# Kernel tuning notes

Hardware: AMD Instinct MI355X
Metric: run time of the kernel (lower is better)

The kernel has to match this reference:

```python
import jax, jax.numpy as jnp
import numpy as np

NEG_INF = -10000.0
ALPHA = 0.2      # LeakyReLU slope
EPS = 1e-5       # LayerNorm eps
B, N, D = 8, 2048, 128


def setup_inputs() -> dict:
    key = jax.random.key(0)
    ks = jax.random.split(key, 8)
    x = jax.random.normal(ks[0], (B, N, D), dtype=jnp.float32)
    adj_bool = jax.random.randint(ks[1], (B, N, N), 0, 2, dtype=jnp.int32)
    node_mask = jax.random.randint(ks[2], (B, N), 0, 2, dtype=jnp.int32)
    s = 1.0 / np.sqrt(D)
    W = jax.random.uniform(ks[3], (D, D), jnp.float32, -s, s)    # fc weight (in->out)
    a_l = jax.random.uniform(ks[4], (D,), jnp.float32, -s, s)    # attn_l weight
    a_r = jax.random.uniform(ks[5], (D,), jnp.float32, -s, s)    # attn_r weight
    gamma = jnp.ones((D,), jnp.float32)                          # LayerNorm weight
    beta = jnp.zeros((D,), jnp.float32)                          # LayerNorm bias
    return {"x": x, "adj_bool": adj_bool, "node_mask": node_mask,
            "W": W, "a_l": a_l, "a_r": a_r, "gamma": gamma, "beta": beta}


def reference(x, adj_bool, node_mask, W, a_l, a_r, gamma, beta):
    m = node_mask.astype(x.dtype)[..., None]           # [B,N,1]
    x = x * m
    h = jnp.einsum('bnd,de->bne', x, W)                # [B,N,D]
    e_l = jnp.einsum('bnd,d->bn', h, a_l)              # [B,N]
    e_r = jnp.einsum('bnd,d->bn', h, a_r)              # [B,N]
    e = e_l[:, :, None] + e_r[:, None, :]              # [B,N,N]
    e = jnp.where(e > 0, e, ALPHA * e)                 # LeakyReLU
    pair = (node_mask[:, :, None] * node_mask[:, None, :]) > 0
    allowed = (adj_bool > 0) & pair
    e = jnp.where(allowed, e, NEG_INF)
    attn = jax.nn.softmax(e, axis=-1)                  # finite (NEG_INF fill), nan_to_num is a no-op
    out = jnp.einsum('bij,bjd->bid', attn, h)          # dropout in eval mode = identity
    out = (out + x) * m                                # residual (ind==outd), then node mask
    mu = jnp.mean(out, axis=-1, keepdims=True)
    var = jnp.var(out, axis=-1, keepdims=True)
    out = (out - mu) * jax.lax.rsqrt(var + EPS) * gamma + beta
    return out
```

## Files before the change

### kernel.cpp

```cpp
#include <hip/hip_runtime.h>
#include <stdint.h>


#define BB 8
#define NN 2048
#define DD 128
#define GAT_NEG_INF -10000.0f
#define LN_EPS 1e-5f

typedef __attribute__((ext_vector_type(8))) short short8;
typedef __attribute__((ext_vector_type(4))) float f32x4;

__device__ __forceinline__ unsigned pk_bf16(float a, float b) {
    unsigned ua = __float_as_uint(a); ua += 0x7FFFu + ((ua >> 16) & 1u);
    unsigned ub = __float_as_uint(b); ub += 0x7FFFu + ((ub >> 16) & 1u);
    return (ua >> 16) | (ub & 0xFFFF0000u);
}
__device__ __forceinline__ unsigned short bf16_rtn(float a) {
    unsigned ua = __float_as_uint(a);
    return (unsigned short)((ua + 0x7FFFu + ((ua >> 16) & 1u)) >> 16);
}

__global__ void prep_wt(const float* __restrict__ W,
                        unsigned short* __restrict__ WThi,
                        unsigned short* __restrict__ WTlo)
{
    int idx = blockIdx.x * 256 + threadIdx.x;
    int k = idx >> 7, n = idx & 127;
    float w = W[idx];
    unsigned short hi = bf16_rtn(w);
    float hif = __uint_as_float((unsigned)hi << 16);
    WThi[n * DD + k] = hi;
    WTlo[n * DD + k] = bf16_rtn(w - hif);
}

__global__ __launch_bounds__(256) void fc_kernel(
    const float* __restrict__ x, const int* __restrict__ mask,
    const unsigned short* __restrict__ WThi, const unsigned short* __restrict__ WTlo,
    const float* __restrict__ a_l, const float* __restrict__ a_r,
    unsigned short* __restrict__ hT, float* __restrict__ el, float* __restrict__ er)
{
    const int t    = threadIdx.x;
    const int wv   = t >> 6;
    const int lane = t & 63;
    const int col  = lane & 15;
    const int grp  = lane >> 4;
    const int b    = blockIdx.x & 7;
    const int it   = blockIdx.x >> 3;
    const int i0   = it * 64 + wv * 16;

    const float* xrow = x + ((size_t)(b * NN + i0 + col)) * DD + grp * 8;
    const float  mm   = (float)mask[b * NN + i0 + col];

    f32x4 acc[8];
#pragma unroll
    for (int nb = 0; nb < 8; ++nb) acc[nb] = (f32x4)0.f;

    union AU { unsigned u[4]; short8 v; };
    union BU { int4 q; short8 v; };

#pragma unroll
    for (int ks = 0; ks < 4; ++ks) {
        float4 xa = *(const float4*)(xrow + ks * 32);
        float4 xb = *(const float4*)(xrow + ks * 32 + 4);
        float xv[8] = {xa.x, xa.y, xa.z, xa.w, xb.x, xb.y, xb.z, xb.w};
        unsigned short hi[8]; float lo[8];
#pragma unroll
        for (int u = 0; u < 8; ++u) {
            float v = xv[u] * mm;
            hi[u] = bf16_rtn(v);
            lo[u] = v - __uint_as_float((unsigned)hi[u] << 16);
        }
        AU Ahi, Alo;
#pragma unroll
        for (int j = 0; j < 4; ++j) {
            Ahi.u[j] = (unsigned)hi[2 * j] | ((unsigned)hi[2 * j + 1] << 16);
            Alo.u[j] = pk_bf16(lo[2 * j], lo[2 * j + 1]);
        }
#pragma unroll
        for (int nb = 0; nb < 8; ++nb) {
            BU Bhi, Blo;
            Bhi.q = *(const int4*)(WThi + (nb * 16 + col) * DD + ks * 32 + grp * 8);
            Blo.q = *(const int4*)(WTlo + (nb * 16 + col) * DD + ks * 32 + grp * 8);
            acc[nb] = __builtin_amdgcn_mfma_f32_16x16x32_bf16(Ahi.v, Bhi.v, acc[nb], 0, 0, 0);
            acc[nb] = __builtin_amdgcn_mfma_f32_16x16x32_bf16(Alo.v, Bhi.v, acc[nb], 0, 0, 0);
            acc[nb] = __builtin_amdgcn_mfma_f32_16x16x32_bf16(Ahi.v, Blo.v, acc[nb], 0, 0, 0);
        }
    }

    float sl[4] = {0.f, 0.f, 0.f, 0.f}, sr[4] = {0.f, 0.f, 0.f, 0.f};
#pragma unroll
    for (int nb = 0; nb < 8; ++nb) {
        float alv = a_l[nb * 16 + col];
        float arv = a_r[nb * 16 + col];
#pragma unroll
        for (int reg = 0; reg < 4; ++reg) {
            sl[reg] += acc[nb][reg] * alv;
            sr[reg] += acc[nb][reg] * arv;
        }
    }
#pragma unroll
    for (int off = 1; off < 16; off <<= 1)
#pragma unroll
        for (int reg = 0; reg < 4; ++reg) {
            sl[reg] += __shfl_xor(sl[reg], off, 64);
            sr[reg] += __shfl_xor(sr[reg], off, 64);
        }
    if (col == 0) {
#pragma unroll
        for (int reg = 0; reg < 4; ++reg) {
            el[b * NN + i0 + grp * 4 + reg] = sl[reg];
            er[b * NN + i0 + grp * 4 + reg] = sr[reg];
        }
    }

#pragma unroll
    for (int nb = 0; nb < 8; ++nb) {
        unsigned p01 = pk_bf16(acc[nb][0], acc[nb][1]);
        unsigned p23 = pk_bf16(acc[nb][2], acc[nb][3]);
        *(uint2*)(hT + ((size_t)(b * DD + nb * 16 + col)) * NN + i0 + grp * 4) =
            make_uint2(p01, p23);
    }
}

__global__ __launch_bounds__(256, 4) void attn_kernel(
    const float* __restrict__ x, const int* __restrict__ adj,
    const int* __restrict__ mask, const unsigned short* __restrict__ hT,
    const float* __restrict__ el, const float* __restrict__ er,
    const float* __restrict__ gamma, const float* __restrict__ beta,
    float* __restrict__ outp)
{
    __shared__ __align__(16) float macc[4][16][132];
    __shared__ float mls[4][16][2];

    const int t    = threadIdx.x;
    const int wv   = t >> 6;
    const int lane = t & 63;
    const int row  = lane & 15;
    const int grp  = lane >> 4;
    const int b    = blockIdx.x & 7;
    const int it   = blockIdx.x >> 3;
    const int i0   = it * 16;
    const int gi   = i0 + row;
    const int j0   = wv * 512;

    const float el_r = el[b * NN + gi];
    const int   mi   = mask[b * NN + gi];
    const int*  adj_row = adj + ((size_t)(b * NN + gi)) * NN + j0;
    const float* er_w = er + b * NN + j0;
    const int*   mk_w = mask + b * NN + j0;
    const unsigned short* hT_b = hT + (size_t)b * DD * NN;

    f32x4 acc[8];
#pragma unroll
    for (int nb = 0; nb < 8; ++nb) acc[nb] = (f32x4)0.f;
    float m_run = -3.0e38f, l_run = 0.f;

    int4 pa0, pa1, pa2, pa3;
    float4 pe0, pe1, pe2, pe3;
    int4 pq0, pq1, pq2, pq3;

    auto load_meta = [&](int jt) {
        const int jb = jt * 64 + grp * 8;
        pa0 = *(const int4*)(adj_row + jb);
        pa1 = *(const int4*)(adj_row + jb + 4);
        pa2 = *(const int4*)(adj_row + jb + 32);
        pa3 = *(const int4*)(adj_row + jb + 36);
        pe0 = *(const float4*)(er_w + jb);
        pe1 = *(const float4*)(er_w + jb + 4);
        pe2 = *(const float4*)(er_w + jb + 32);
        pe3 = *(const float4*)(er_w + jb + 36);
        pq0 = *(const int4*)(mk_w + jb);
        pq1 = *(const int4*)(mk_w + jb + 4);
        pq2 = *(const int4*)(mk_w + jb + 32);
        pq3 = *(const int4*)(mk_w + jb + 36);
    };
    load_meta(0);

    union BU { int4 q; short8 v; };
    union AU { unsigned u[4]; short8 v; };

#pragma unroll 1
    for (int jt = 0; jt < 8; ++jt) {
        int4 a0 = pa0, a1 = pa1, a2 = pa2, a3 = pa3;
        float4 e0 = pe0, e1 = pe1, e2 = pe2, e3 = pe3;
        int4 q0 = pq0, q1 = pq1, q2 = pq2, q3 = pq3;
        load_meta(jt < 7 ? jt + 1 : jt);

        BU bf[16];
        {
            const int jb = j0 + jt * 64 + grp * 8;
#pragma unroll
            for (int s = 0; s < 2; ++s)
#pragma unroll
                for (int nb = 0; nb < 8; ++nb)
                    bf[s * 8 + nb].q = *(const int4*)(hT_b
                        + (size_t)(nb * 16 + row) * NN + jb + s * 32);
        }

        int   av[16] = {a0.x,a0.y,a0.z,a0.w, a1.x,a1.y,a1.z,a1.w,
                        a2.x,a2.y,a2.z,a2.w, a3.x,a3.y,a3.z,a3.w};
        int   qv[16] = {q0.x,q0.y,q0.z,q0.w, q1.x,q1.y,q1.z,q1.w,
                        q2.x,q2.y,q2.z,q2.w, q3.x,q3.y,q3.z,q3.w};
        float ev[16] = {e0.x,e0.y,e0.z,e0.w, e1.x,e1.y,e1.z,e1.w,
                        e2.x,e2.y,e2.z,e2.w, e3.x,e3.y,e3.z,e3.w};
        float ss[16];
        float tmax = -3.0e38f;
#pragma unroll
        for (int u = 0; u < 16; ++u) {
            float e = el_r + ev[u];
            e = fmaxf(e, 0.2f * e);
            bool ok = (av[u] & qv[u] & mi) != 0;
            ss[u] = ok ? e : GAT_NEG_INF;
            tmax = fmaxf(tmax, ss[u]);
        }
        tmax = fmaxf(tmax, __shfl_xor(tmax, 16, 64));
        tmax = fmaxf(tmax, __shfl_xor(tmax, 32, 64));
        float m_new = fmaxf(m_run, tmax);
        float al    = __expf(m_run - m_new);
        float p[16];
        float psum = 0.f;
#pragma unroll
        for (int u = 0; u < 16; ++u) {
            p[u] = __expf(ss[u] - m_new);
            psum += p[u];
        }
        psum += __shfl_xor(psum, 16, 64);
        psum += __shfl_xor(psum, 32, 64);
        l_run = l_run * al + psum;
        m_run = m_new;

        float alr[4];
#pragma unroll
        for (int reg = 0; reg < 4; ++reg) alr[reg] = __shfl(al, grp * 4 + reg, 64);
#pragma unroll
        for (int nb = 0; nb < 8; ++nb) {
            acc[nb][0] *= alr[0]; acc[nb][1] *= alr[1];
            acc[nb][2] *= alr[2]; acc[nb][3] *= alr[3];
        }

        AU A0, A1;
#pragma unroll
        for (int k = 0; k < 4; ++k) {
            A0.u[k] = pk_bf16(p[2 * k],     p[2 * k + 1]);
            A1.u[k] = pk_bf16(p[8 + 2 * k], p[8 + 2 * k + 1]);
        }
#pragma unroll
        for (int nb = 0; nb < 8; ++nb)
            acc[nb] = __builtin_amdgcn_mfma_f32_16x16x32_bf16(A0.v, bf[nb].v, acc[nb], 0, 0, 0);
#pragma unroll
        for (int nb = 0; nb < 8; ++nb)
            acc[nb] = __builtin_amdgcn_mfma_f32_16x16x32_bf16(A1.v, bf[8 + nb].v, acc[nb], 0, 0, 0);
    }

    if (grp == 0) { mls[wv][row][0] = m_run; mls[wv][row][1] = l_run; }
#pragma unroll
    for (int nb = 0; nb < 8; ++nb)
#pragma unroll
        for (int reg = 0; reg < 4; ++reg)
            macc[wv][grp * 4 + reg][nb * 16 + row] = acc[nb][reg];
    __syncthreads();

    const float g0  = gamma[2 * lane], g1 = gamma[2 * lane + 1];
    const float be0 = beta[2 * lane],  be1 = beta[2 * lane + 1];
#pragma unroll
    for (int q = 0; q < 4; ++q) {
        const int r  = wv * 4 + q;
        const int gir = i0 + r;
        float m0 = mls[0][r][0], m1 = mls[1][r][0], m2 = mls[2][r][0], m3 = mls[3][r][0];
        float m_f = fmaxf(fmaxf(m0, m1), fmaxf(m2, m3));
        float sc0 = __expf(m0 - m_f), sc1 = __expf(m1 - m_f);
        float sc2 = __expf(m2 - m_f), sc3 = __expf(m3 - m_f);
        float l_f = mls[0][r][1] * sc0 + mls[1][r][1] * sc1
                  + mls[2][r][1] * sc2 + mls[3][r][1] * sc3;
        float inv = 1.0f / l_f;
        float2 v0 = *(const float2*)&macc[0][r][2 * lane];
        float2 v1 = *(const float2*)&macc[1][r][2 * lane];
        float2 v2 = *(const float2*)&macc[2][r][2 * lane];
        float2 v3 = *(const float2*)&macc[3][r][2 * lane];
        float ox = v0.x * sc0 + v1.x * sc1 + v2.x * sc2 + v3.x * sc3;
        float oy = v0.y * sc0 + v1.y * sc1 + v2.y * sc2 + v3.y * sc3;

        float mq = (float)mask[b * NN + gir];
        float2 xv = *(const float2*)(x + ((size_t)(b * NN + gir)) * DD + 2 * lane);
        float w0 = (ox * inv + xv.x) * mq;
        float w1 = (oy * inv + xv.y) * mq;

        float s1 = w0 + w1, s2 = w0 * w0 + w1 * w1;
#pragma unroll
        for (int off = 32; off; off >>= 1) {
            s1 += __shfl_xor(s1, off, 64);
            s2 += __shfl_xor(s2, off, 64);
        }
        float mu  = s1 * (1.0f / DD);
        float var = s2 * (1.0f / DD) - mu * mu;
        float rsd = rsqrtf(var + LN_EPS);
        *(float2*)(outp + ((size_t)(b * NN + gir)) * DD + 2 * lane) =
            make_float2((w0 - mu) * rsd * g0 + be0, (w1 - mu) * rsd * g1 + be1);
    }
}

extern "C" void kernel_launch(void* const* d_in, const int* in_sizes, int n_in,
                              void* d_out, int out_size, void* d_ws, size_t ws_size,
                              hipStream_t stream) {
    const float* x     = (const float*)d_in[0];
    const int*   adj   = (const int*)d_in[1];
    const int*   maskp = (const int*)d_in[2];
    const float* W     = (const float*)d_in[3];
    const float* a_l   = (const float*)d_in[4];
    const float* a_r   = (const float*)d_in[5];
    const float* gamma = (const float*)d_in[6];
    const float* beta  = (const float*)d_in[7];
    float*       outp  = (float*)d_out;

    unsigned short* hT = (unsigned short*)d_ws;
    float* el = (float*)(hT + (size_t)BB * DD * NN);
    float* er = el + (size_t)BB * NN;
    unsigned short* WThi = (unsigned short*)(er + (size_t)BB * NN);
    unsigned short* WTlo = WThi + DD * DD;

    prep_wt<<<64, 256, 0, stream>>>(W, WThi, WTlo);
    fc_kernel<<<BB * (NN / 64), 256, 0, stream>>>(x, maskp, WThi, WTlo,
                                                  a_l, a_r, hT, el, er);
    attn_kernel<<<BB * (NN / 16), 256, 0, stream>>>(x, adj, maskp, hT, el, er,
                                                    gamma, beta, outp);
}
```

Baseline: 280.3 us.

## Precompute adjacency and node mask as packed bitmask before attention kernel

Adds a prep kernel that streams the int32 adjacency matrix and the column node mask once and packs `adj & mask_j & mask_i` into 64-bit words, one bit per edge. The attention kernel then loads one 64-bit word per tile instead of 16 int4 adjacency and mask loads per lane, and tests bits with shifts. This is meant to cut global-memory loads, register pressure and latency inside the compute-heavy attention loop. The cost is an extra launch that still reads the full adjacency matrix, plus a small bitmask buffer in workspace.

```diff
diff --git a/kernel.cpp b/kernel.cpp
--- a/kernel.cpp
+++ b/kernel.cpp
@@ -32,6 +32,29 @@
     float hif = __uint_as_float((unsigned)hi << 16);
     WThi[n * DD + k] = hi;
     WTlo[n * DD + k] = bf16_rtn(w - hif);
+}
+
+__global__ __launch_bounds__(256) void prep_adj(
+    const int* __restrict__ adj, const int* __restrict__ mask,
+    unsigned long long* __restrict__ bits)
+{
+    int gid  = blockIdx.x * 256 + threadIdx.x;
+    int word = gid & 31;
+    int row  = (gid >> 5) & 2047;
+    int b    = gid >> 16;
+    const int* abase = adj + ((size_t)(b * NN + row)) * NN + word * 64;
+    const int* mbase = mask + b * NN + word * 64;
+    int mi = mask[b * NN + row];
+    unsigned long long w = 0ull;
+#pragma unroll
+    for (int g = 0; g < 16; ++g) {
+        int4 a = *(const int4*)(abase + g * 4);
+        int4 m = *(const int4*)(mbase + g * 4);
+        unsigned nib = (unsigned)((a.x & m.x) | ((a.y & m.y) << 1)
+                                | ((a.z & m.z) << 2) | ((a.w & m.w) << 3));
+        w |= (unsigned long long)nib << (g * 4);
+    }
+    bits[gid] = mi ? w : 0ull;
 }
 
 __global__ __launch_bounds__(256) void fc_kernel(
@@ -124,7 +147,7 @@
 }
 
 __global__ __launch_bounds__(256, 4) void attn_kernel(
-    const float* __restrict__ x, const int* __restrict__ adj,
+    const float* __restrict__ x, const unsigned long long* __restrict__ bits,
     const int* __restrict__ mask, const unsigned short* __restrict__ hT,
     const float* __restrict__ el, const float* __restrict__ er,
     const float* __restrict__ gamma, const float* __restrict__ beta,
@@ -145,10 +168,9 @@
     const int j0   = wv * 512;
 
     const float el_r = el[b * NN + gi];
-    const int   mi   = mask[b * NN + gi];
-    const int*  adj_row = adj + ((size_t)(b * NN + gi)) * NN + j0;
+    const unsigned long long* bitsrow = bits + ((size_t)(b * NN + gi)) * 32 + wv * 8;
     const float* er_w = er + b * NN + j0;
-    const int*   mk_w = mask + b * NN + j0;
+    const int*   mk_b = mask + b * NN;
     const unsigned short* hT_b = hT + (size_t)b * DD * NN;
 
     f32x4 acc[8];
@@ -156,24 +178,16 @@
     for (int nb = 0; nb < 8; ++nb) acc[nb] = (f32x4)0.f;
     float m_run = -3.0e38f, l_run = 0.f;
 
-    int4 pa0, pa1, pa2, pa3;
     float4 pe0, pe1, pe2, pe3;
-    int4 pq0, pq1, pq2, pq3;
+    unsigned long long pw;
 
     auto load_meta = [&](int jt) {
         const int jb = jt * 64 + grp * 8;
-        pa0 = *(const int4*)(adj_row + jb);
-        pa1 = *(const int4*)(adj_row + jb + 4);
-        pa2 = *(const int4*)(adj_row + jb + 32);
-        pa3 = *(const int4*)(adj_row + jb + 36);
         pe0 = *(const float4*)(er_w + jb);
         pe1 = *(const float4*)(er_w + jb + 4);
         pe2 = *(const float4*)(er_w + jb + 32);
         pe3 = *(const float4*)(er_w + jb + 36);
-        pq0 = *(const int4*)(mk_w + jb);
-        pq1 = *(const int4*)(mk_w + jb + 4);
-        pq2 = *(const int4*)(mk_w + jb + 32);
-        pq3 = *(const int4*)(mk_w + jb + 36);
+        pw  = bitsrow[jt];
     };
     load_meta(0);
 
@@ -182,9 +196,8 @@
 
 #pragma unroll 1
     for (int jt = 0; jt < 8; ++jt) {
-        int4 a0 = pa0, a1 = pa1, a2 = pa2, a3 = pa3;
         float4 e0 = pe0, e1 = pe1, e2 = pe2, e3 = pe3;
-        int4 q0 = pq0, q1 = pq1, q2 = pq2, q3 = pq3;
+        unsigned long long w = pw;
         load_meta(jt < 7 ? jt + 1 : jt);
 
         BU bf[16];
@@ -198,10 +211,10 @@
                         + (size_t)(nb * 16 + row) * NN + jb + s * 32);
         }
 
-        int   av[16] = {a0.x,a0.y,a0.z,a0.w, a1.x,a1.y,a1.z,a1.w,
-                        a2.x,a2.y,a2.z,a2.w, a3.x,a3.y,a3.z,a3.w};
-        int   qv[16] = {q0.x,q0.y,q0.z,q0.w, q1.x,q1.y,q1.z,q1.w,
-                        q2.x,q2.y,q2.z,q2.w, q3.x,q3.y,q3.z,q3.w};
+        unsigned lo = (unsigned)(w & 0xffffffffu);
+        unsigned hi = (unsigned)(w >> 32);
+        unsigned b16 = ((lo >> (grp * 8)) & 0xffu) | ((((hi >> (grp * 8)) & 0xffu)) << 8);
+
         float ev[16] = {e0.x,e0.y,e0.z,e0.w, e1.x,e1.y,e1.z,e1.w,
                         e2.x,e2.y,e2.z,e2.w, e3.x,e3.y,e3.z,e3.w};
         float ss[16];
@@ -210,8 +223,7 @@
         for (int u = 0; u < 16; ++u) {
             float e = el_r + ev[u];
             e = fmaxf(e, 0.2f * e);
-            bool ok = (av[u] & qv[u] & mi) != 0;
-            ss[u] = ok ? e : GAT_NEG_INF;
+            ss[u] = ((b16 >> u) & 1u) ? e : GAT_NEG_INF;
             tmax = fmaxf(tmax, ss[u]);
         }
         tmax = fmaxf(tmax, __shfl_xor(tmax, 16, 64));
@@ -281,7 +293,7 @@
         float ox = v0.x * sc0 + v1.x * sc1 + v2.x * sc2 + v3.x * sc3;
         float oy = v0.y * sc0 + v1.y * sc1 + v2.y * sc2 + v3.y * sc3;
 
-        float mq = (float)mask[b * NN + gir];
+        float mq = (float)mk_b[gir];
         float2 xv = *(const float2*)(x + ((size_t)(b * NN + gir)) * DD + 2 * lane);
         float w0 = (ox * inv + xv.x) * mq;
         float w1 = (oy * inv + xv.y) * mq;
@@ -318,10 +330,12 @@
     float* er = el + (size_t)BB * NN;
     unsigned short* WThi = (unsigned short*)(er + (size_t)BB * NN);
     unsigned short* WTlo = WThi + DD * DD;
+    unsigned long long* bits = (unsigned long long*)(WTlo + DD * DD);
 
     prep_wt<<<64, 256, 0, stream>>>(W, WThi, WTlo);
+    prep_adj<<<2048, 256, 0, stream>>>(adj, maskp, bits);
     fc_kernel<<<BB * (NN / 64), 256, 0, stream>>>(x, maskp, WThi, WTlo,
                                                   a_l, a_r, hT, el, er);
-    attn_kernel<<<BB * (NN / 16), 256, 0, stream>>>(x, adj, maskp, hT, el, er,
+    attn_kernel<<<BB * (NN / 16), 256, 0, stream>>>(x, bits, maskp, hT, el, er,
                                                     gamma, beta, outp);
 }
```

Result: slower. 318.7 us (+13.7%).
